# Optimization experiments

Measured on AMD Instinct MI355X. Metric: run time of the kernel, lower is better.

The kernel has to match this reference:

```python
import jax, jax.numpy as jnp
import numpy as np

D_MODEL = 1024

def setup_inputs() -> dict:
    key = jax.random.key(0)
    ks = jax.random.split(key, 7)
    B, T, D = 4, 4096, D_MODEL
    s = 1.0 / np.sqrt(D)
    return {
        "x": jax.random.normal(ks[0], (B, T, D), dtype=jnp.float32),
        "Wq": jax.random.normal(ks[1], (D, D), dtype=jnp.float32) * s,
        "bq": jax.random.normal(ks[2], (D,), dtype=jnp.float32) * 0.01,
        "Wk": jax.random.normal(ks[3], (D, D), dtype=jnp.float32) * s,
        "bk": jax.random.normal(ks[4], (D,), dtype=jnp.float32) * 0.01,
        "Wv": jax.random.normal(ks[5], (D, D), dtype=jnp.float32) * s,
        "bv": jax.random.normal(ks[6], (D,), dtype=jnp.float32) * 0.01,
    }

def reference(x, Wq, bq, Wk, bk, Wv, bv):
    # x: [B, T, D]; Linear weights stored [out, in] like torch -> x @ W.T + b
    D = x.shape[-1]
    T = x.shape[1]
    scale = jnp.sqrt(jnp.asarray(D, dtype=x.dtype))
    Q = jnp.einsum('btd,ed->bte', x, Wq) + bq
    K = jnp.einsum('btd,ed->bte', x, Wk) + bk
    V = jnp.einsum('btd,ed->bte', x, Wv) + bv
    scores = jnp.einsum('bqd,bkd->bqk', Q, K) / scale  # [B, T, T]
    causal = jnp.tril(jnp.ones((T, T), dtype=bool))    # True = keep (q >= k)
    neg_inf = jnp.asarray(-jnp.inf, dtype=scores.dtype)
    scores = jnp.where(causal, scores, neg_inf)
    probs = jax.nn.softmax(scores, axis=-1)
    return jnp.einsum('bqk,bkd->bqd', probs, V)
```

## Files before the change

kernel.cpp:

```cpp
#include <hip/hip_runtime.h>
#include <hip/hip_bf16.h>
#include <math.h>


typedef __bf16 bf16;
typedef __bf16 bf16x8 __attribute__((ext_vector_type(8)));
typedef float  f32x4  __attribute__((ext_vector_type(4)));

#define LOG2E 1.4426950408889634f

static constexpr size_t OFF_XB   = 0;
static constexpr size_t OFF_WQB  = 33554432;
static constexpr size_t OFF_WKB  = 35651584;
static constexpr size_t OFF_WVB  = 37748736;
static constexpr size_t OFF_Q    = 39845888;
static constexpr size_t OFF_K    = 73400320;
static constexpr size_t OFF_VT   = 106954752;
static constexpr size_t OFF_S    = 140509184;
static constexpr size_t OFF_PSUM = 209715200;
static constexpr size_t OFF_LINV = 211812352;

typedef __attribute__((address_space(1))) void gvoid_t;
typedef __attribute__((address_space(3))) void lvoid_t;

__device__ __forceinline__ void gload16(const void* g, void* l) {
  __builtin_amdgcn_global_load_lds((gvoid_t*)g, (lvoid_t*)l, 16, 0, 0);
}

#define PRIO1() __builtin_amdgcn_s_setprio(1)
#define PRIO0() __builtin_amdgcn_s_setprio(0)
#define BARF()  asm volatile("s_barrier" ::: "memory")
#define SB0()   __builtin_amdgcn_sched_barrier(0)
#define VM0()   asm volatile("s_waitcnt vmcnt(0)" ::: "memory")
#define VM4()   asm volatile("s_waitcnt vmcnt(4)" ::: "memory")

struct Ctx { int tid, lane, quad, col16, wr, wc, wcol; };
__device__ __forceinline__ Ctx mk_ctx() {
  Ctx c; c.tid = (int)threadIdx.x; c.lane = c.tid & 63;
  int w = c.tid >> 6;
  c.quad = c.lane >> 4; c.col16 = c.lane & 15;
  c.wr = (w >> 1) * 64; c.wc = (w & 1) * 64; c.wcol = w & 1;
  return c;
}

__device__ __forceinline__ void stage_tile(const bf16* g, long ld, bf16* s, int tid) {
  int lane = tid & 63, w = tid >> 6;
  const bf16* gp = g + (long)(lane >> 2) * ld + (long)(lane & 3) * 8;
  long step = 16 * ld;
  gload16(gp + (long)(2 * w) * step,     s + (2 * w) * 512);
  gload16(gp + (long)(2 * w + 1) * step, s + (2 * w + 1) * 512);
}

__device__ __forceinline__ void mfma_step(const bf16* sA, const bf16* sB,
                                          const Ctx& c, f32x4 acc[4][4]) {
  bf16x8 a[4], b[4];
#pragma unroll
  for (int i = 0; i < 4; ++i) {
    a[i] = *(const bf16x8*)(sA + ((c.wr + i * 16 + c.col16) * 32 + c.quad * 8));
    b[i] = *(const bf16x8*)(sB + ((c.wc + i * 16 + c.col16) * 32 + c.quad * 8));
  }
#pragma unroll
  for (int i = 0; i < 4; ++i)
#pragma unroll
    for (int j = 0; j < 4; ++j)
      acc[i][j] = __builtin_amdgcn_mfma_f32_16x16x32_bf16(a[i], b[j], acc[i][j], 0, 0, 0);
}

__device__ __forceinline__ void zero_acc(f32x4 acc[4][4]) {
  f32x4 z = {0.f, 0.f, 0.f, 0.f};
#pragma unroll
  for (int i = 0; i < 4; ++i)
#pragma unroll
    for (int j = 0; j < 4; ++j) acc[i][j] = z;
}

__device__ __forceinline__ int tridec(int i) {
  int qt = (int)((sqrtf(8.0f * (float)i + 1.0f) - 1.0f) * 0.5f);
  while ((qt + 1) * (qt + 2) / 2 <= i) ++qt;
  while (qt * (qt + 1) / 2 > i) --qt;
  return qt;
}

struct CC { int soff, ra0, ra1, rb0, rb1, lofs; };
__device__ __forceinline__ CC mk_cc(int tid) {
  CC c;
  int lane = tid & 63, w = tid >> 6;
  int quad = lane >> 4, col16 = lane & 15;
  int wrow = (w >> 2) << 7, wcol = (w & 3) << 6;
  int c7 = col16 & 7;
  c.soff = ((tid >> 3) << 10) + (((tid & 7) ^ ((tid >> 3) & 7)) << 3);
  c.ra0 = ((wrow + col16) << 6) + ((quad ^ c7) << 3);
  c.ra1 = ((wrow + col16) << 6) + (((4 | quad) ^ c7) << 3);
  c.rb0 = ((wcol + col16) << 6) + ((quad ^ c7) << 3);
  c.rb1 = ((wcol + col16) << 6) + (((4 | quad) ^ c7) << 3);
  c.lofs = w << 9;
  return c;
}

__device__ __forceinline__ void stg(const bf16* g, int kofs, bf16* l, const CC& c) {
  const bf16* g0 = g + kofs + c.soff;
  gload16(g0,         l + c.lofs);
  gload16(g0 + 65536, l + c.lofs + 4096);
}

__device__ __forceinline__ void read_a(const bf16* buf, const CC& c, int h, bf16x8 a[8]) {
#pragma unroll
  for (int f = 0; f < 4; ++f) {
    a[f * 2 + 0] = *(const bf16x8*)(buf + c.ra0 + h * 4096 + f * 1024);
    a[f * 2 + 1] = *(const bf16x8*)(buf + c.ra1 + h * 4096 + f * 1024);
  }
}

__device__ __forceinline__ void read_b(const bf16* buf, const CC& c, int cc, bf16x8 bb[4]) {
#pragma unroll
  for (int g = 0; g < 2; ++g) {
    bb[g * 2 + 0] = *(const bf16x8*)(buf + c.rb0 + cc * 2048 + g * 1024);
    bb[g * 2 + 1] = *(const bf16x8*)(buf + c.rb1 + cc * 2048 + g * 1024);
  }
}

__device__ __forceinline__ void read_ab(const bf16* bufA, const bf16* bufB,
                                        const CC& c, bf16x8 a[8], bf16x8 bb[4]) {
#pragma unroll
  for (int f = 0; f < 4; ++f) {
    a[f * 2 + 0] = *(const bf16x8*)(bufA + c.ra0 + f * 1024);
    a[f * 2 + 1] = *(const bf16x8*)(bufA + c.ra1 + f * 1024);
    if (f < 2) {
      bb[f * 2 + 0] = *(const bf16x8*)(bufB + c.rb0 + f * 1024);
      bb[f * 2 + 1] = *(const bf16x8*)(bufB + c.rb1 + f * 1024);
    }
  }
}

__device__ __forceinline__ void mfma16(const bf16x8 a[8], const bf16x8 bb[4],
                                       int h, int cc, f32x4 acc[8][4]) {
#pragma unroll
  for (int f = 0; f < 4; ++f)
#pragma unroll
    for (int g = 0; g < 2; ++g)
#pragma unroll
      for (int kk = 0; kk < 2; ++kk)
        acc[h * 4 + f][cc * 2 + g] = __builtin_amdgcn_mfma_f32_16x16x32_bf16(
            a[f * 2 + kk], bb[g * 2 + kk], acc[h * 4 + f][cc * 2 + g], 0, 0, 0);
}

__device__ __forceinline__ void zero8x4(f32x4 acc[8][4]) {
  f32x4 z = {0.f, 0.f, 0.f, 0.f};
#pragma unroll
  for (int i = 0; i < 8; ++i)
#pragma unroll
    for (int j = 0; j < 4; ++j) acc[i][j] = z;
}

template <int NT>
__device__ __forceinline__ void gemm256_core(const bf16* __restrict__ Ag,
                                             const bf16* __restrict__ Bg,
                                             bf16* sA0, bf16* sA1,
                                             bf16* sB0, bf16* sB1,
                                             const CC& c, f32x4 acc[8][4]) {
  stg(Ag, 0,           sA0, c); stg(Ag, 131072,      sA0 + 8192, c);
  stg(Bg, 0,           sB0, c); stg(Bg, 131072,      sB0 + 8192, c);
  stg(Bg, 64,          sB1, c); stg(Bg, 64 + 131072, sB1 + 8192, c);
  VM4();

  bf16x8 a[8], b0[4], b1[4];
#pragma unroll 1
  for (int i = 0; i < NT / 2 - 1; ++i) {
    const int k1 = (2 * i + 1) << 6, k2 = k1 + 64, k3 = k1 + 128;
    BARF();
    read_ab(sA0, sB0, c, a, b0);
    stg(Ag, k1, sA1, c);
    PRIO1(); mfma16(a, b0, 0, 0, acc); PRIO0(); SB0();
    BARF();
    read_b(sB0, c, 1, b1);
    stg(Ag, k1 + 131072, sA1 + 8192, c);
    PRIO1(); mfma16(a, b1, 0, 1, acc); PRIO0(); SB0();
    BARF();
    read_a(sA0, c, 1, a);
    stg(Bg, k2, sB0, c);
    PRIO1(); mfma16(a, b1, 1, 1, acc); PRIO0(); SB0();
    BARF();
    stg(Bg, k2 + 131072, sB0 + 8192, c);
    PRIO1(); mfma16(a, b0, 1, 0, acc); PRIO0();
    VM4(); SB0();
    BARF();
    read_ab(sA1, sB1, c, a, b0);
    stg(Ag, k2, sA0, c);
    PRIO1(); mfma16(a, b0, 0, 0, acc); PRIO0(); SB0();
    BARF();
    read_b(sB1, c, 1, b1);
    stg(Ag, k2 + 131072, sA0 + 8192, c);
    PRIO1(); mfma16(a, b1, 0, 1, acc); PRIO0(); SB0();
    BARF();
    read_a(sA1, c, 1, a);
    stg(Bg, k3, sB1, c);
    PRIO1(); mfma16(a, b1, 1, 1, acc); PRIO0(); SB0();
    BARF();
    stg(Bg, k3 + 131072, sB1 + 8192, c);
    PRIO1(); mfma16(a, b0, 1, 0, acc); PRIO0();
    VM4(); SB0();
  }
  {
    const int k1 = (NT - 1) << 6;
    BARF();
    read_ab(sA0, sB0, c, a, b0);
    stg(Ag, k1, sA1, c);
    PRIO1(); mfma16(a, b0, 0, 0, acc); PRIO0(); SB0();
    BARF();
    read_b(sB0, c, 1, b1);
    stg(Ag, k1 + 131072, sA1 + 8192, c);
    PRIO1(); mfma16(a, b1, 0, 1, acc); PRIO0(); SB0();
    BARF();
    read_a(sA0, c, 1, a);
    PRIO1(); mfma16(a, b1, 1, 1, acc); PRIO0(); SB0();
    PRIO1(); mfma16(a, b0, 1, 0, acc); PRIO0();
    VM0(); SB0();
    BARF();
    read_ab(sA1, sB1, c, a, b0);
    PRIO1(); mfma16(a, b0, 0, 0, acc); PRIO0(); SB0();
    BARF();
    read_b(sB1, c, 1, b1);
    PRIO1(); mfma16(a, b1, 0, 1, acc); PRIO0(); SB0();
    BARF();
    read_a(sA1, c, 1, a);
    PRIO1(); mfma16(a, b1, 1, 1, acc); PRIO0();
    mfma16(a, b0, 1, 0, acc);
  }
}


__global__ __launch_bounds__(256) void cvt_all(const float* __restrict__ x,
                                               const float* __restrict__ Wq,
                                               const float* __restrict__ Wk,
                                               const float* __restrict__ Wv,
                                               bf16* __restrict__ xb,
                                               bf16* __restrict__ wqb,
                                               bf16* __restrict__ wkb,
                                               bf16* __restrict__ wvb) {
  int b = (int)blockIdx.x;
  const float* in; bf16* out; long base;
  if (b < 8192)      { in = x;  out = xb;  base = (long)b * 2048; }
  else if (b < 8704) { in = Wq; out = wqb; base = (long)(b - 8192) * 2048; }
  else if (b < 9216) { in = Wk; out = wkb; base = (long)(b - 8704) * 2048; }
  else               { in = Wv; out = wvb; base = (long)(b - 9216) * 2048; }
  long i = base + (long)threadIdx.x * 8;
  float4 f0 = *(const float4*)(in + i);
  float4 f1 = *(const float4*)(in + i + 4);
  bf16x8 h;
  h[0] = (bf16)f0.x; h[1] = (bf16)f0.y; h[2] = (bf16)f0.z; h[3] = (bf16)f0.w;
  h[4] = (bf16)f1.x; h[5] = (bf16)f1.y; h[6] = (bf16)f1.z; h[7] = (bf16)f1.w;
  *(bf16x8*)(out + i) = h;
}

__global__ __launch_bounds__(512, 2) void qkv_gemm(const bf16* __restrict__ X,
                                                   const bf16* __restrict__ Wq,
                                                   const bf16* __restrict__ Wk,
                                                   const bf16* __restrict__ Wv,
                                                   const float* __restrict__ bq,
                                                   const float* __restrict__ bk,
                                                   const float* __restrict__ bv,
                                                   bf16* __restrict__ Q,
                                                   bf16* __restrict__ K,
                                                   bf16* __restrict__ Vt) {
  __shared__ __align__(16) bf16 lds[4][16384];
  const int tid = (int)threadIdx.x;
  const CC c = mk_cc(tid);
  int b0i = (int)blockIdx.x;
  int b = (b0i & 7) * 96 + (b0i >> 3);
  const bf16 *Ag, *Bg;
  const bool is_vt = (b >= 512);
  if (!is_vt) {
    int isK = b >> 8, rem = b & 255;
    Ag = X + (long)(rem >> 2) * 262144;
    Bg = (isK ? Wk : Wq) + (long)(rem & 3) * 262144;
  } else {
    int rem = b - 512;
    Ag = Wv + (long)((rem >> 4) & 3) * 262144;
    Bg = X + (long)(rem >> 6) * 4194304 + (long)(rem & 15) * 262144;
  }
  f32x4 acc[8][4];
  zero8x4(acc);
  gemm256_core<16>(Ag, Bg, lds[0], lds[1], lds[2], lds[3], c, acc);

  const int lane = tid & 63, w = tid >> 6;
  const int quad = lane >> 4, col16 = lane & 15;
  const int wrow = (w >> 2) << 7, wcol = (w & 3) << 6;
  if (!is_vt) {
    int isK = b >> 8, rem = b & 255;
    long r0 = (long)(rem >> 2) * 256, c0 = (long)(rem & 3) * 256;
    const float* bias = isK ? bk : bq;
    bf16* out = isK ? K : Q;
#pragma unroll
    for (int n = 0; n < 4; ++n) {
      int col = (int)c0 + wcol + (n >> 1) * 32 + (n & 1) * 16 + col16;
      float bb = bias[col];
#pragma unroll
      for (int m = 0; m < 8; ++m) {
        long rowb = r0 + wrow + (m >> 2) * 64 + (m & 3) * 16 + quad * 4;
#pragma unroll
        for (int r = 0; r < 4; ++r)
          out[(rowb + r) * 1024 + col] = (bf16)(acc[m][n][r] + bb);
      }
    }
  } else {
    int rem = b - 512;
    int z = rem >> 6;
    long r0 = (long)((rem >> 4) & 3) * 256, c0 = (long)(rem & 15) * 256;
    bf16* out = Vt + (long)z * 4194304;
#pragma unroll
    for (int m = 0; m < 8; ++m) {
      long rowb = r0 + wrow + (m >> 2) * 64 + (m & 3) * 16 + quad * 4;
      float bb[4];
#pragma unroll
      for (int r = 0; r < 4; ++r) bb[r] = bv[rowb + r];
#pragma unroll
      for (int n = 0; n < 4; ++n) {
        int col = (int)c0 + wcol + (n >> 1) * 32 + (n & 1) * 16 + col16;
#pragma unroll
        for (int r = 0; r < 4; ++r)
          out[(rowb + r) * 4096 + col] = (bf16)(acc[m][n][r] + bb[r]);
      }
    }
  }
}

__global__ __launch_bounds__(512, 2) void s_gemm(const bf16* __restrict__ Q,
                                                 const bf16* __restrict__ K,
                                                 bf16* __restrict__ S,
                                                 float* __restrict__ psum) {
  __shared__ __align__(16) bf16 lds[4][16384];
  __shared__ float sred[8][128];
  const int tid = (int)threadIdx.x;
  const CC c = mk_cc(tid);
  int b0i = (int)blockIdx.x;
  int b = (b0i & 7) * 68 + (b0i >> 3);
  int z = b & 3, ti = b >> 2;
  int QT = tridec(ti);
  int KT = ti - QT * (QT + 1) / 2;
  const bf16* Ag = Q + (long)z * 4194304 + (long)QT * 262144;
  const bf16* Bg = K + (long)z * 4194304 + (long)KT * 262144;
  f32x4 acc[8][4];
  zero8x4(acc);
  gemm256_core<16>(Ag, Bg, lds[0], lds[1], lds[2], lds[3], c, acc);

  const int lane = tid & 63, w = tid >> 6;
  const int quad = lane >> 4, col16 = lane & 15;
  const int rh = w >> 2, ch = (w & 3) >> 1;
  const int wcol64 = (w & 1) << 6;
  const bool diag = (QT == KT);
  const bool skip = diag && (rh == 0) && (ch == 1);
  const bool mask = diag && (rh == ch);
  const int qt128 = 2 * QT + rh, kt128 = 2 * KT + ch;
  bf16* st = S + ((long)z * 528 + (long)(qt128 * (qt128 + 1) / 2 + kt128)) * 16384;
  float rs[8][4];
#pragma unroll
  for (int m = 0; m < 8; ++m)
#pragma unroll
    for (int r = 0; r < 4; ++r) rs[m][r] = 0.f;
#pragma unroll
  for (int m = 0; m < 8; ++m) {
    int row_l = (m >> 2) * 64 + (m & 3) * 16 + quad * 4;
#pragma unroll
    for (int n = 0; n < 4; ++n) {
      int col_l = wcol64 + (n >> 1) * 32 + (n & 1) * 16 + col16;
#pragma unroll
      for (int r = 0; r < 4; ++r) {
        float p = exp2f(acc[m][n][r] * (0.03125f * LOG2E));
        if (mask && col_l > row_l + r) p = 0.0f;
        bf16 h = (bf16)p;
        if (!skip) st[(row_l + r) * 128 + col_l] = h;
        rs[m][r] += (float)h;
      }
    }
  }
#pragma unroll
  for (int m = 0; m < 8; ++m)
#pragma unroll
    for (int r = 0; r < 4; ++r)
#pragma unroll
      for (int msk = 1; msk <= 8; msk <<= 1)
        rs[m][r] += __shfl_xor(rs[m][r], msk);
  if (col16 == 0) {
#pragma unroll
    for (int m = 0; m < 8; ++m)
#pragma unroll
      for (int r = 0; r < 4; ++r)
        sred[w][(m >> 2) * 64 + (m & 3) * 16 + quad * 4 + r] = rs[m][r];
  }
  __syncthreads();
  {
    int rh2 = (tid >> 7) & 1, row_l = tid & 127, ch2 = tid >> 8;
    int base = rh2 * 4 + ch2 * 2;
    psum[((long)z * 4096 + (long)QT * 256 + rh2 * 128 + row_l) * 32 + 2 * KT + ch2] =
        sred[base][row_l] + sred[base + 1][row_l];
  }
}

__global__ __launch_bounds__(256) void inv_sums(const float* __restrict__ psum,
                                                float* __restrict__ linv) {
  long i = (long)blockIdx.x * 256 + threadIdx.x;
  int q = (int)(i & 4095);
  int nt = (q >> 7) + 1;
  const float* ps = psum + i * 32;
  float l = 0.f;
  for (int t = 0; t < nt; ++t) l += ps[t];
  linv[i] = 1.0f / l;
}

__global__ __launch_bounds__(256) void o_gemm(const bf16* __restrict__ S,
                                              const bf16* __restrict__ Vt,
                                              const float* __restrict__ linv,
                                              float* __restrict__ out) {
  __shared__ __align__(16) bf16 sA[2][128 * 32], sB[2][128 * 32];
  Ctx c = mk_ctx();
  int b = (int)blockIdx.x;
  int z = b & 3, et = (b >> 2) & 7, q0i = (b >> 5) & 7, gen = b >> 8;
  int qt = (gen == 0) ? q0i : (gen == 1) ? 15 - q0i
         : (gen == 2) ? 16 + q0i : 31 - q0i;
  long q0 = (long)qt * 128, e0 = (long)et * 128;
  const bf16* Bb = Vt + (long)z * 4194304 + e0 * 4096;
  long tribase = ((long)z * 528 + (long)qt * (qt + 1) / 2) * 16384;
  f32x4 acc[4][4]; zero_acc(acc);
  int kend = (qt + 1) * 128;
  for (int k = 0; k < kend; k += 64) {
    const bf16* Ab = S + tribase + (long)(k >> 7) * 16384 + (k & 127);
    stage_tile(Ab,      128, sA[0], c.tid);
    stage_tile(Ab + 32, 128, sA[1], c.tid);
    stage_tile(Bb + k,      4096, sB[0], c.tid);
    stage_tile(Bb + k + 32, 4096, sB[1], c.tid);
    __syncthreads();
    mfma_step(sA[0], sB[0], c, acc);
    mfma_step(sA[1], sB[1], c, acc);
    __syncthreads();
  }
  long zq = (long)z * 4096 + q0;
#pragma unroll
  for (int i = 0; i < 4; ++i) {
    int rowb = c.wr + i * 16 + c.quad * 4;
    float li[4];
#pragma unroll
    for (int r = 0; r < 4; ++r) li[r] = linv[zq + rowb + r];
#pragma unroll
    for (int j = 0; j < 4; ++j) {
      int col = c.wc + j * 16 + c.col16;
#pragma unroll
      for (int r = 0; r < 4; ++r)
        out[(zq + rowb + r) * 1024 + e0 + col] = acc[i][j][r] * li[r];
    }
  }
}

extern "C" void kernel_launch(void* const* d_in, const int* in_sizes, int n_in,
                              void* d_out, int out_size, void* d_ws, size_t ws_size,
                              hipStream_t stream) {
  (void)in_sizes; (void)n_in; (void)out_size; (void)ws_size;
  const float* x  = (const float*)d_in[0];
  const float* Wq = (const float*)d_in[1];
  const float* bq = (const float*)d_in[2];
  const float* Wk = (const float*)d_in[3];
  const float* bk = (const float*)d_in[4];
  const float* Wv = (const float*)d_in[5];
  const float* bv = (const float*)d_in[6];

  char* ws = (char*)d_ws;
  bf16*  xb   = (bf16*)(ws + OFF_XB);
  bf16*  wqb  = (bf16*)(ws + OFF_WQB);
  bf16*  wkb  = (bf16*)(ws + OFF_WKB);
  bf16*  wvb  = (bf16*)(ws + OFF_WVB);
  bf16*  Qb   = (bf16*)(ws + OFF_Q);
  bf16*  Kb   = (bf16*)(ws + OFF_K);
  bf16*  Vtb  = (bf16*)(ws + OFF_VT);
  bf16*  Sb   = (bf16*)(ws + OFF_S);
  float* psum = (float*)(ws + OFF_PSUM);
  float* linv = (float*)(ws + OFF_LINV);

  cvt_all<<<9728, 256, 0, stream>>>(x, Wq, Wk, Wv, xb, wqb, wkb, wvb);
  qkv_gemm<<<768, 512, 0, stream>>>(xb, wqb, wkb, wvb, bq, bk, bv, Qb, Kb, Vtb);
  s_gemm<<<544, 512, 0, stream>>>(Qb, Kb, Sb, psum);
  inv_sums<<<64, 256, 0, stream>>>(psum, linv);
  o_gemm<<<1024, 256, 0, stream>>>(Sb, Vtb, linv, (float*)d_out);
}
```

Baseline: 486.0 us.

## Change LDS swizzle pattern and pack s_gemm tiles into 512 blocks

Replaces the XOR-based LDS swizzle with a simpler two-bit pattern, using one base offset plus a +32 element offset for the second k-half of the fragment reads. It also launches s_gemm with 512 blocks instead of 544, and the first 32 blocks loop to handle the extra 32 tiles. The aim is to fit the grid into a single wave of resident blocks (256 CUs, 2 blocks each) and to trim address arithmetic. The risk is that the new swizzle raises LDS bank conflicts, and the 32 blocks doing two tiles lengthen the tail.

```diff
diff --git a/kernel.cpp b/kernel.cpp
--- a/kernel.cpp
+++ b/kernel.cpp
@@ -81,18 +81,16 @@
   return qt;
 }
 
-struct CC { int soff, ra0, ra1, rb0, rb1, lofs; };
+struct CC { int soff, rA, rB, lofs; };
 __device__ __forceinline__ CC mk_cc(int tid) {
   CC c;
   int lane = tid & 63, w = tid >> 6;
   int quad = lane >> 4, col16 = lane & 15;
   int wrow = (w >> 2) << 7, wcol = (w & 3) << 6;
-  int c7 = col16 & 7;
-  c.soff = ((tid >> 3) << 10) + (((tid & 7) ^ ((tid >> 3) & 7)) << 3);
-  c.ra0 = ((wrow + col16) << 6) + ((quad ^ c7) << 3);
-  c.ra1 = ((wrow + col16) << 6) + (((4 | quad) ^ c7) << 3);
-  c.rb0 = ((wcol + col16) << 6) + ((quad ^ c7) << 3);
-  c.rb1 = ((wcol + col16) << 6) + (((4 | quad) ^ c7) << 3);
+  c.soff = ((tid >> 3) << 10) + (((tid & 7) ^ (((tid >> 5) & 1) << 1)) << 3);
+  int cS = (quad << 3) ^ (((col16 >> 2) & 1) << 4);
+  c.rA = ((wrow + col16) << 6) + cS;
+  c.rB = ((wcol + col16) << 6) + cS;
   c.lofs = w << 9;
   return c;
 }
@@ -106,16 +104,16 @@
 __device__ __forceinline__ void read_a(const bf16* buf, const CC& c, int h, bf16x8 a[8]) {
 #pragma unroll
   for (int f = 0; f < 4; ++f) {
-    a[f * 2 + 0] = *(const bf16x8*)(buf + c.ra0 + h * 4096 + f * 1024);
-    a[f * 2 + 1] = *(const bf16x8*)(buf + c.ra1 + h * 4096 + f * 1024);
+    a[f * 2 + 0] = *(const bf16x8*)(buf + c.rA + h * 4096 + f * 1024);
+    a[f * 2 + 1] = *(const bf16x8*)(buf + c.rA + h * 4096 + f * 1024 + 32);
   }
 }
 
 __device__ __forceinline__ void read_b(const bf16* buf, const CC& c, int cc, bf16x8 bb[4]) {
 #pragma unroll
   for (int g = 0; g < 2; ++g) {
-    bb[g * 2 + 0] = *(const bf16x8*)(buf + c.rb0 + cc * 2048 + g * 1024);
-    bb[g * 2 + 1] = *(const bf16x8*)(buf + c.rb1 + cc * 2048 + g * 1024);
+    bb[g * 2 + 0] = *(const bf16x8*)(buf + c.rB + cc * 2048 + g * 1024);
+    bb[g * 2 + 1] = *(const bf16x8*)(buf + c.rB + cc * 2048 + g * 1024 + 32);
   }
 }
 
@@ -123,11 +121,11 @@
                                         const CC& c, bf16x8 a[8], bf16x8 bb[4]) {
 #pragma unroll
   for (int f = 0; f < 4; ++f) {
-    a[f * 2 + 0] = *(const bf16x8*)(bufA + c.ra0 + f * 1024);
-    a[f * 2 + 1] = *(const bf16x8*)(bufA + c.ra1 + f * 1024);
+    a[f * 2 + 0] = *(const bf16x8*)(bufA + c.rA + f * 1024);
+    a[f * 2 + 1] = *(const bf16x8*)(bufA + c.rA + f * 1024 + 32);
     if (f < 2) {
-      bb[f * 2 + 0] = *(const bf16x8*)(bufB + c.rb0 + f * 1024);
-      bb[f * 2 + 1] = *(const bf16x8*)(bufB + c.rb1 + f * 1024);
+      bb[f * 2 + 0] = *(const bf16x8*)(bufB + c.rB + f * 1024);
+      bb[f * 2 + 1] = *(const bf16x8*)(bufB + c.rB + f * 1024 + 32);
     }
   }
 }
@@ -332,67 +330,73 @@
   __shared__ float sred[8][128];
   const int tid = (int)threadIdx.x;
   const CC c = mk_cc(tid);
-  int b0i = (int)blockIdx.x;
-  int b = (b0i & 7) * 68 + (b0i >> 3);
-  int z = b & 3, ti = b >> 2;
-  int QT = tridec(ti);
-  int KT = ti - QT * (QT + 1) / 2;
-  const bf16* Ag = Q + (long)z * 4194304 + (long)QT * 262144;
-  const bf16* Bg = K + (long)z * 4194304 + (long)KT * 262144;
-  f32x4 acc[8][4];
-  zero8x4(acc);
-  gemm256_core<16>(Ag, Bg, lds[0], lds[1], lds[2], lds[3], c, acc);
-
-  const int lane = tid & 63, w = tid >> 6;
-  const int quad = lane >> 4, col16 = lane & 15;
-  const int rh = w >> 2, ch = (w & 3) >> 1;
-  const int wcol64 = (w & 1) << 6;
-  const bool diag = (QT == KT);
-  const bool skip = diag && (rh == 0) && (ch == 1);
-  const bool mask = diag && (rh == ch);
-  const int qt128 = 2 * QT + rh, kt128 = 2 * KT + ch;
-  bf16* st = S + ((long)z * 528 + (long)(qt128 * (qt128 + 1) / 2 + kt128)) * 16384;
-  float rs[8][4];
-#pragma unroll
-  for (int m = 0; m < 8; ++m)
-#pragma unroll
-    for (int r = 0; r < 4; ++r) rs[m][r] = 0.f;
-#pragma unroll
-  for (int m = 0; m < 8; ++m) {
-    int row_l = (m >> 2) * 64 + (m & 3) * 16 + quad * 4;
-#pragma unroll
-    for (int n = 0; n < 4; ++n) {
-      int col_l = wcol64 + (n >> 1) * 32 + (n & 1) * 16 + col16;
-#pragma unroll
-      for (int r = 0; r < 4; ++r) {
-        float p = exp2f(acc[m][n][r] * (0.03125f * LOG2E));
-        if (mask && col_l > row_l + r) p = 0.0f;
-        bf16 h = (bf16)p;
-        if (!skip) st[(row_l + r) * 128 + col_l] = h;
-        rs[m][r] += (float)h;
+  const int r = (int)blockIdx.x;
+  const int nit = (r < 32) ? 2 : 1;
+#pragma unroll 1
+  for (int it = 0; it < nit; ++it) {
+    int b = (it == 0) ? ((r & 7) * 64 + (r >> 3))
+                      : (512 + r);
+    int z = b & 3, ti = b >> 2;
+    int QT = tridec(ti);
+    int KT = ti - QT * (QT + 1) / 2;
+    const bf16* Ag = Q + (long)z * 4194304 + (long)QT * 262144;
+    const bf16* Bg = K + (long)z * 4194304 + (long)KT * 262144;
+    f32x4 acc[8][4];
+    zero8x4(acc);
+    gemm256_core<16>(Ag, Bg, lds[0], lds[1], lds[2], lds[3], c, acc);
+
+    const int lane = tid & 63, w = tid >> 6;
+    const int quad = lane >> 4, col16 = lane & 15;
+    const int rh = w >> 2, ch = (w & 3) >> 1;
+    const int wcol64 = (w & 1) << 6;
+    const bool diag = (QT == KT);
+    const bool skip = diag && (rh == 0) && (ch == 1);
+    const bool mask = diag && (rh == ch);
+    const int qt128 = 2 * QT + rh, kt128 = 2 * KT + ch;
+    bf16* st = S + ((long)z * 528 + (long)(qt128 * (qt128 + 1) / 2 + kt128)) * 16384;
+    float rs[8][4];
+#pragma unroll
+    for (int m = 0; m < 8; ++m)
+#pragma unroll
+      for (int rr = 0; rr < 4; ++rr) rs[m][rr] = 0.f;
+#pragma unroll
+    for (int m = 0; m < 8; ++m) {
+      int row_l = (m >> 2) * 64 + (m & 3) * 16 + quad * 4;
+#pragma unroll
+      for (int n = 0; n < 4; ++n) {
+        int col_l = wcol64 + (n >> 1) * 32 + (n & 1) * 16 + col16;
+#pragma unroll
+        for (int rr = 0; rr < 4; ++rr) {
+          float p = exp2f(acc[m][n][rr] * (0.03125f * LOG2E));
+          if (mask && col_l > row_l + rr) p = 0.0f;
+          bf16 h = (bf16)p;
+          if (!skip) st[(row_l + rr) * 128 + col_l] = h;
+          rs[m][rr] += (float)h;
+        }
       }
     }
-  }
-#pragma unroll
-  for (int m = 0; m < 8; ++m)
-#pragma unroll
-    for (int r = 0; r < 4; ++r)
-#pragma unroll
-      for (int msk = 1; msk <= 8; msk <<= 1)
-        rs[m][r] += __shfl_xor(rs[m][r], msk);
-  if (col16 == 0) {
 #pragma unroll
     for (int m = 0; m < 8; ++m)
 #pragma unroll
-      for (int r = 0; r < 4; ++r)
-        sred[w][(m >> 2) * 64 + (m & 3) * 16 + quad * 4 + r] = rs[m][r];
-  }
-  __syncthreads();
-  {
-    int rh2 = (tid >> 7) & 1, row_l = tid & 127, ch2 = tid >> 8;
-    int base = rh2 * 4 + ch2 * 2;
-    psum[((long)z * 4096 + (long)QT * 256 + rh2 * 128 + row_l) * 32 + 2 * KT + ch2] =
-        sred[base][row_l] + sred[base + 1][row_l];
+      for (int rr = 0; rr < 4; ++rr)
+#pragma unroll
+        for (int msk = 1; msk <= 8; msk <<= 1)
+          rs[m][rr] += __shfl_xor(rs[m][rr], msk);
+    if (col16 == 0) {
+#pragma unroll
+      for (int m = 0; m < 8; ++m)
+#pragma unroll
+        for (int rr = 0; rr < 4; ++rr)
+          sred[w][(m >> 2) * 64 + (m & 3) * 16 + quad * 4 + rr] = rs[m][rr];
+    }
+    __syncthreads();
+    {
+      int rh2 = (tid >> 7) & 1, row_l = tid & 127, ch2 = tid >> 8;
+      int base = rh2 * 4 + ch2 * 2;
+      psum[((long)z * 4096 + (long)QT * 256 + rh2 * 128 + row_l) * 32 + 2 * KT + ch2] =
+          sred[base][row_l] + sred[base + 1][row_l];
+    }
+    if (it + 1 < nit) __syncthreads();
   }
 }
 
@@ -476,7 +480,7 @@
 
   cvt_all<<<9728, 256, 0, stream>>>(x, Wq, Wk, Wv, xb, wqb, wkb, wvb);
   qkv_gemm<<<768, 512, 0, stream>>>(xb, wqb, wkb, wvb, bq, bk, bv, Qb, Kb, Vtb);
-  s_gemm<<<544, 512, 0, stream>>>(Qb, Kb, Sb, psum);
+  s_gemm<<<512, 512, 0, stream>>>(Qb, Kb, Sb, psum);
   inv_sums<<<64, 256, 0, stream>>>(psum, linv);
   o_gemm<<<1024, 256, 0, stream>>>(Sb, Vtb, linv, (float*)d_out);
 }
```

New measurement: 527.9 us. +8.6%, slower.
